# Optimization experiments

Hardware: AMD Instinct MI355X
Metric: run time of the kernel (lower is better)

## Reference

```python
import jax, jax.numpy as jnp
import numpy as np
import math

DIM = 64
N_, H_, W_ = 8, 64, 64
EPS = 1e-5


def setup_inputs() -> dict:
    key = jax.random.key(0)
    ks = jax.random.split(key, 11)
    c = DIM
    s = 1.0 / math.sqrt(c)
    x = jax.random.normal(ks[0], (N_, c, H_, W_), dtype=jnp.float32)
    return {
        "x": x,
        "gamma": jnp.ones((c,), jnp.float32),
        "beta": jnp.zeros((c,), jnp.float32),
        "wq": jax.random.normal(ks[1], (c, c), jnp.float32) * s,
        "bq": jax.random.normal(ks[2], (c,), jnp.float32) * 0.01,
        "wk": jax.random.normal(ks[3], (c, c), jnp.float32) * s,
        "bk": jax.random.normal(ks[4], (c,), jnp.float32) * 0.01,
        "wv": jax.random.normal(ks[5], (c, c), jnp.float32) * s,
        "bv": jax.random.normal(ks[6], (c,), jnp.float32) * 0.01,
        "wo": jax.random.normal(ks[7], (c, c), jnp.float32) * s,
        "bo": jax.random.normal(ks[8], (c,), jnp.float32) * 0.01,
    }


def _conv1x1(x, w, b):
    # 1x1 conv == channel mixing: x [n,c,h,w], w [out,in], b [out]
    return jnp.einsum('nchw,oc->nohw', x, w) + b[None, :, None, None]


def _batchnorm(x, gamma, beta):
    # training-mode BatchNorm2d: biased batch stats over (N,H,W)
    mean = jnp.mean(x, axis=(0, 2, 3), keepdims=True)
    var = jnp.var(x, axis=(0, 2, 3), keepdims=True)
    xn = (x - mean) * jax.lax.rsqrt(var + EPS)
    return xn * gamma[None, :, None, None] + beta[None, :, None, None]


def reference(x, gamma, beta, wq, bq, wk, bk, wv, bv, wo, bo):
    n, c, h, w = x.shape
    hw = h * w
    norm_x = _batchnorm(x, gamma, beta)
    q = _conv1x1(norm_x, wq, bq).reshape(n, c, hw)  # [n,c,hw]
    k = _conv1x1(norm_x, wk, bk).reshape(n, c, hw)  # [n,c,hw]
    v = _conv1x1(norm_x, wv, bv).reshape(n, c, hw)  # [n,c,hw]
    # scores [n, hw, hw] = q^T k / sqrt(c) -- full N x N matrix (memory bound)
    scores = jnp.einsum('nci,ncj->nij', q, k) / math.sqrt(c)
    attn = jax.nn.softmax(scores, axis=-1)
    # res [n, hw, c] = attn @ v^T
    res = jnp.einsum('nij,ncj->nic', attn, v)
    # faithful to original: raw reshape [n,hw,c] -> [n,c,h,w] (no transpose)
    res = res.reshape(n, c, h, w)
    res = _conv1x1(res, wo, bo)
    return x + res
```

## Files before the change

### kernel.cpp

```cpp
#include <hip/hip_runtime.h>


#define HW 4096
#define CC 64
#define NBATCH 8
#define SPLIT 2
#define TSTEPS 32
#define QSCALE 0.18033688011112042f

using f32x4 = __attribute__((ext_vector_type(4))) float;
using bf16x8 = __attribute__((ext_vector_type(8))) short;
using u32x2 = __attribute__((ext_vector_type(2))) unsigned int;
typedef unsigned short u16;
typedef unsigned int u32;

#if __has_builtin(__builtin_amdgcn_exp2f)
#define EXP2F(v) __builtin_amdgcn_exp2f(v)
#else
#define EXP2F(v) exp2f(v)
#endif

#define MFMA16(a, b, c) __builtin_amdgcn_mfma_f32_16x16x32_bf16(a, b, c, 0, 0, 0)
#define GLDS(gsrc, ldst)                                              \
  __builtin_amdgcn_global_load_lds(                                   \
      (const __attribute__((address_space(1))) void*)(gsrc),          \
      (__attribute__((address_space(3))) void*)(ldst), 16, 0, 0)

__device__ __forceinline__ u16 f2bf(float v) {
  u32 u = __float_as_uint(v);
  return (u16)((u + 0x7fffu + ((u >> 16) & 1u)) >> 16);
}
__device__ __forceinline__ float bf2f(u16 h) {
  return __uint_as_float(((u32)h) << 16);
}
__device__ __forceinline__ u32 cvtpk_bf16(float lo, float hi) {
  u32 r;
  asm("v_cvt_pk_bf16_f32 %0, %1, %2" : "=v"(r) : "v"(lo), "v"(hi));
  return r;
}

__global__ __launch_bounds__(256) void k_stats1(const float* __restrict__ x,
                                                float* __restrict__ SACC) {
  const int n = blockIdx.x >> 6;
  const int c = blockIdx.x & 63;
  const int tid = threadIdx.x;
  const float* xp = x + ((size_t)n * CC + c) * HW;
  float s1 = 0.f, s2 = 0.f;
#pragma unroll
  for (int i = tid; i < HW; i += 256) {
    const float v = xp[i];
    s1 += v;
    s2 += v * v;
  }
#pragma unroll
  for (int m = 1; m <= 32; m <<= 1) {
    s1 += __shfl_xor(s1, m);
    s2 += __shfl_xor(s2, m);
  }
  __shared__ float r1[4], r2[4];
  const int w = tid >> 6;
  if ((tid & 63) == 0) { r1[w] = s1; r2[w] = s2; }
  __syncthreads();
  if (tid == 0) {
    unsafeAtomicAdd(SACC + c, r1[0] + r1[1] + r1[2] + r1[3]);
    unsafeAtomicAdd(SACC + CC + c, r2[0] + r2[1] + r2[2] + r2[3]);
  }
}

__device__ __forceinline__ void mm16(const float* __restrict__ W,
                                     const float* __restrict__ B,
                                     const float* xcol, int o0, float scale,
                                     float* outv) {
#pragma unroll
  for (int oo = 0; oo < 16; ++oo) {
    const int o = o0 + oo;
    float a = B[o];
#pragma unroll
    for (int c = 0; c < CC; ++c) a = fmaf(W[o * CC + c], xcol[c], a);
    outv[oo] = a * scale;
  }
}

__device__ __forceinline__ void split_store16(const float* v16, u16* dh, u16* dl) {
  u32 hi[8], lo[8];
#pragma unroll
  for (int e = 0; e < 8; ++e) {
    const u16 h0 = f2bf(v16[2 * e]), h1 = f2bf(v16[2 * e + 1]);
    const float l0 = v16[2 * e] - bf2f(h0);
    const float l1 = v16[2 * e + 1] - bf2f(h1);
    hi[e] = (u32)h0 | ((u32)h1 << 16);
    lo[e] = (u32)f2bf(l0) | ((u32)f2bf(l1) << 16);
  }
  ((uint4*)dh)[0] = *(const uint4*)&hi[0];
  ((uint4*)dh)[1] = *(const uint4*)&hi[4];
  ((uint4*)dl)[0] = *(const uint4*)&lo[0];
  ((uint4*)dl)[1] = *(const uint4*)&lo[4];
}

__global__ __launch_bounds__(256) void k_qkv(
    const float* __restrict__ x, const float* __restrict__ SACC,
    const float* __restrict__ gamma, const float* __restrict__ beta,
    const float* __restrict__ wq, const float* __restrict__ bq,
    const float* __restrict__ wk, const float* __restrict__ bk,
    const float* __restrict__ wv, const float* __restrict__ bv,
    u16* __restrict__ QH, u16* __restrict__ QL, u16* __restrict__ KH,
    u16* __restrict__ KL, u16* __restrict__ V) {
  const int n = blockIdx.x >> 6;
  const int i0 = (blockIdx.x & 63) << 6;
  __shared__ float xn[CC][64];
  __shared__ float sa[CC], sb[CC];
  const int tid = threadIdx.x;
  if (tid < CC) {
    const float inv = 1.0f / (float)(NBATCH * HW);
    const float mean = SACC[tid] * inv;
    const float var = SACC[CC + tid] * inv - mean * mean;
    const float a = rsqrtf(var + 1e-5f) * gamma[tid];
    sa[tid] = a;
    sb[tid] = beta[tid] - mean * a;
  }
  __syncthreads();
  {
    const int p = tid & 63;
    const int c0 = (tid >> 6) << 4;
    const float* xp = x + (size_t)n * CC * HW + i0 + p;
#pragma unroll
    for (int cc = 0; cc < 16; ++cc) {
      const int c = c0 + cc;
      xn[c][p] = fmaf(xp[(size_t)c * HW], sa[c], sb[c]);
    }
  }
  __syncthreads();
  const int w = __builtin_amdgcn_readfirstlane(tid >> 6);
  const int p = tid & 63;
  float xcol[CC];
#pragma unroll
  for (int c = 0; c < CC; ++c) xcol[c] = xn[c][p];

  const size_t row = (size_t)n * HW + i0 + p;
  float v16[16];
  mm16(wq, bq, xcol, w * 16, QSCALE, v16);
  split_store16(v16, QH + row * CC + w * 16, QL + row * CC + w * 16);
  mm16(wk, bk, xcol, w * 16, 1.0f, v16);
  split_store16(v16, KH + row * CC + w * 16, KL + row * CC + w * 16);
  mm16(wv, bv, xcol, w * 16, 1.0f, v16);
#pragma unroll
  for (int oo = 0; oo < 16; ++oo)
    V[((size_t)n * CC + w * 16 + oo) * HW + i0 + p] = f2bf(v16[oo]);
}

__global__ __launch_bounds__(256, 2) void k_attn(
    const u16* __restrict__ QH, const u16* __restrict__ QL,
    const u16* __restrict__ KH, const u16* __restrict__ KL,
    const u16* __restrict__ V, float* __restrict__ RES,
    float* __restrict__ Z) {
  const int bid = blockIdx.x;
  const int n = bid & 7;
  const int qt = (bid >> 3) & 31;
  const int s = bid >> 8;
  const int tid = threadIdx.x;
  const int w = tid >> 6;
  const int l = tid & 63;
  const int l15 = l & 15;
  const int lg = l >> 4;
  const int qw0 = qt * 128 + w * 32;
  const int key0 = s * (TSTEPS * 64);

  __shared__ alignas(16) u16 KHs[2][64][64];
  __shared__ alignas(16) u16 KLs[2][64][64];
  __shared__ alignas(16) u16 Vs[2][64][64];
  __shared__ alignas(16) u16 P[4][32][64];

  const int lr8 = l >> 3;
  const u32 eoff = (u32)(((l & 7) * 8) ^ (lr8 << 3));
  const u16* sp[6];
  u16* d0[6];
  u16* d1[6];
  size_t stp[6];
#pragma unroll
  for (int c = 0; c < 6; ++c) {
    const int idx = w * 6 + c;
    const int tile = idx >> 3;
    const int j = idx & 7;
    const int lrow = j * 8 + lr8;
    if (tile == 0) {
      sp[c] = KH + ((size_t)n * HW + key0 + lrow) * CC + eoff;
      stp[c] = (size_t)64 * CC;
      d0[c] = &KHs[0][j * 8][0];
      d1[c] = &KHs[1][j * 8][0];
    } else if (tile == 1) {
      sp[c] = KL + ((size_t)n * HW + key0 + lrow) * CC + eoff;
      stp[c] = (size_t)64 * CC;
      d0[c] = &KLs[0][j * 8][0];
      d1[c] = &KLs[1][j * 8][0];
    } else {
      sp[c] = V + ((size_t)n * CC + lrow) * HW + key0 + eoff;
      stp[c] = 64;
      d0[c] = &Vs[0][j * 8][0];
      d1[c] = &Vs[1][j * 8][0];
    }
  }
  auto stage = [&](int bufsel) {
#pragma unroll
    for (int c = 0; c < 6; ++c) {
      u16* dst = bufsel ? d1[c] : d0[c];
      GLDS(sp[c], dst);
      sp[c] += stp[c];
    }
  };

  bf16x8 qh[2][2], ql[2][2];
  {
    const size_t qbase = ((size_t)n * HW + qw0 + l15) * CC + lg * 8;
#pragma unroll
    for (int qb = 0; qb < 2; ++qb)
#pragma unroll
      for (int m = 0; m < 2; ++m) {
        const size_t off = qbase + (size_t)qb * 16 * CC + m * 32;
        qh[qb][m] = *(const bf16x8*)(QH + off);
        ql[qb][m] = *(const bf16x8*)(QL + off);
      }
  }

  f32x4 acc[2][4];
#pragma unroll
  for (int qb = 0; qb < 2; ++qb)
#pragma unroll
    for (int chb = 0; chb < 4; ++chb)
      acc[qb][chb] = (f32x4){0.f, 0.f, 0.f, 0.f};
  float zacc[2] = {0.f, 0.f};

  stage(0);
  asm volatile("s_waitcnt vmcnt(0)\n\ts_barrier" ::: "memory");

  const int swz = (l15 & 7) << 4;
  char* const Pw = (char*)&P[w][0][0];

#pragma unroll 1
  for (int t = 0; t < TSTEPS; ++t) {
    const int buf = t & 1;
    if (t + 1 < TSTEPS) stage(buf ^ 1);
    const char* khb = (const char*)&KHs[buf][0][0];
    const char* klb = (const char*)&KLs[buf][0][0];
    const char* vsb = (const char*)&Vs[buf][0][0];

    f32x4 sc[2][4];
#pragma unroll
    for (int kb = 0; kb < 4; ++kb) {
      const int rb = (kb * 16 + l15) * 128;
      const int c0 = (lg * 16) ^ swz;
      const int c1 = (64 + lg * 16) ^ swz;
      const bf16x8 kh0 = *(const bf16x8*)(khb + rb + c0);
      const bf16x8 kh1 = *(const bf16x8*)(khb + rb + c1);
      const bf16x8 kl0 = *(const bf16x8*)(klb + rb + c0);
      const bf16x8 kl1 = *(const bf16x8*)(klb + rb + c1);
      __builtin_amdgcn_s_setprio(1);
#pragma unroll
      for (int qb = 0; qb < 2; ++qb) {
        f32x4 s4 = {0.f, 0.f, 0.f, 0.f};
        s4 = MFMA16(kh0, qh[qb][0], s4);
        s4 = MFMA16(kh1, qh[qb][1], s4);
        s4 = MFMA16(kh0, ql[qb][0], s4);
        s4 = MFMA16(kh1, ql[qb][1], s4);
        s4 = MFMA16(kl0, qh[qb][0], s4);
        s4 = MFMA16(kl1, qh[qb][1], s4);
        sc[qb][kb] = s4;
      }
      __builtin_amdgcn_s_setprio(0);
    }
#pragma unroll
    for (int qb = 0; qb < 2; ++qb) {
      char* const prow = Pw + (qb * 16 + l15) * 128;
      float zs = 0.f;
#pragma unroll
      for (int kb = 0; kb < 4; ++kb) {
        const float p0 = EXP2F(sc[qb][kb][0]);
        const float p1 = EXP2F(sc[qb][kb][1]);
        const float p2 = EXP2F(sc[qb][kb][2]);
        const float p3 = EXP2F(sc[qb][kb][3]);
        zs += (p0 + p1) + (p2 + p3);
        const u32x2 pk = {cvtpk_bf16(p0, p1), cvtpk_bf16(p2, p3)};
        *(u32x2*)(prow + ((kb * 32 + lg * 8) ^ swz)) = pk;
      }
      zacc[qb] += zs;
    }
#pragma unroll
    for (int m2 = 0; m2 < 2; ++m2) {
      const int cc2 = (m2 * 64 + lg * 16) ^ swz;
      bf16x8 vb[4];
#pragma unroll
      for (int chb = 0; chb < 4; ++chb)
        vb[chb] = *(const bf16x8*)(vsb + (chb * 16 + l15) * 128 + cc2);
      __builtin_amdgcn_s_setprio(1);
#pragma unroll
      for (int qb = 0; qb < 2; ++qb) {
        const bf16x8 pa = *(const bf16x8*)(Pw + (qb * 16 + l15) * 128 + cc2);
#pragma unroll
        for (int chb = 0; chb < 4; ++chb)
          acc[qb][chb] = MFMA16(pa, vb[chb], acc[qb][chb]);
      }
      __builtin_amdgcn_s_setprio(0);
    }
    asm volatile("s_waitcnt vmcnt(0) lgkmcnt(0)\n\ts_barrier" ::: "memory");
  }

#pragma unroll
  for (int qb = 0; qb < 2; ++qb) {
    zacc[qb] += __shfl_xor(zacc[qb], 16);
    zacc[qb] += __shfl_xor(zacc[qb], 32);
  }
  if (l < 16) {
    unsafeAtomicAdd(Z + (size_t)n * HW + qw0 + l, zacc[0]);
    unsafeAtomicAdd(Z + (size_t)n * HW + qw0 + 16 + l, zacc[1]);
  }
  float* resn = RES + ((size_t)n * HW + qw0) * CC;
#pragma unroll
  for (int qb = 0; qb < 2; ++qb)
#pragma unroll
    for (int r = 0; r < 4; ++r) {
      const int row = qb * 16 + lg * 4 + r;
#pragma unroll
      for (int chb = 0; chb < 4; ++chb)
        unsafeAtomicAdd(resn + (size_t)row * CC + chb * 16 + l15,
                        acc[qb][chb][r]);
    }
}

__global__ __launch_bounds__(256) void k_out(const float* __restrict__ RES,
                                             const float* __restrict__ Z,
                                             const float* __restrict__ x,
                                             const float* __restrict__ wo,
                                             const float* __restrict__ bo,
                                             float* __restrict__ out) {
  const int n = blockIdx.x >> 6;
  const int j = ((blockIdx.x & 63) << 6) + (threadIdx.x & 63);
  const int oq = __builtin_amdgcn_readfirstlane(threadIdx.x >> 6);
  const float* rn = RES + (size_t)n * HW * CC;
  const float* zb = Z + (size_t)n * HW;
  const int jh = j >> 6;
  float rcol[CC];
#pragma unroll
  for (int c2 = 0; c2 < CC; ++c2)
    rcol[c2] = rn[(size_t)c2 * HW + j] * (1.0f / zb[c2 * 64 + jh]);
  const size_t xb = (size_t)n * CC * HW;
  for (int o = oq * 16; o < oq * 16 + 16; ++o) {
    float sacc = bo[o];
#pragma unroll
    for (int c2 = 0; c2 < CC; ++c2)
      sacc = fmaf(wo[o * CC + c2], rcol[c2], sacc);
    out[xb + (size_t)o * HW + j] = x[xb + (size_t)o * HW + j] + sacc;
  }
}

extern "C" void kernel_launch(void* const* d_in, const int* in_sizes, int n_in,
                              void* d_out, int out_size, void* d_ws,
                              size_t ws_size, hipStream_t stream) {
  const float* x = (const float*)d_in[0];
  const float* gamma = (const float*)d_in[1];
  const float* beta = (const float*)d_in[2];
  const float* wq = (const float*)d_in[3];
  const float* bq = (const float*)d_in[4];
  const float* wk = (const float*)d_in[5];
  const float* bk = (const float*)d_in[6];
  const float* wv = (const float*)d_in[7];
  const float* bv = (const float*)d_in[8];
  const float* wo = (const float*)d_in[9];
  const float* bo = (const float*)d_in[10];
  float* out = (float*)d_out;

  char* ws = (char*)d_ws;
  float* SACC = (float*)ws;
  float* Z = (float*)(ws + 1024);
  float* RES = (float*)(ws + 1024 + (size_t)NBATCH * HW * 4);
  const size_t INIT_BYTES =
      1024 + (size_t)NBATCH * HW * 4 + (size_t)NBATCH * HW * CC * 4;
  const size_t ARR = (size_t)NBATCH * HW * CC;
  u16* QH = (u16*)(ws + INIT_BYTES);
  u16* QL = QH + ARR;
  u16* KH = QL + ARR;
  u16* KL = KH + ARR;
  u16* V = KL + ARR;

  hipMemsetAsync(ws, 0, INIT_BYTES, stream);
  hipLaunchKernelGGL(k_stats1, dim3(512), dim3(256), 0, stream, x, SACC);
  hipLaunchKernelGGL(k_qkv, dim3(512), dim3(256), 0, stream, x, SACC, gamma,
                     beta, wq, bq, wk, bk, wv, bv, QH, QL, KH, KL, V);
  hipLaunchKernelGGL(k_attn, dim3(512), dim3(256), 0, stream, QH, QL, KH, KL,
                     V, RES, Z);
  hipLaunchKernelGGL(k_out, dim3(512), dim3(256), 0, stream, RES, Z, x, wo, bo,
                     out);
}
```

Baseline: 232.1 us.

## Split attention keys four ways, load V directly to registers, coalesce QK stores

Splits the key range into four chunks instead of two, which doubles the attention grid to 1024 blocks and raises the occupancy target to three blocks per SM. V tiles are now loaded straight from global memory into registers rather than staged through shared memory, which frees LDS and drops the V staging work. In the QKV kernel, the Q/K hi/lo values are transposed through shared memory so each row is written with coalesced 16-byte stores. The costs are more atomic traffic on Z and RES partial sums, and exposed global-load latency for V inside the loop.

```diff
diff --git a/kernel.cpp b/kernel.cpp
--- a/kernel.cpp
+++ b/kernel.cpp
@@ -4,8 +4,8 @@
 #define HW 4096
 #define CC 64
 #define NBATCH 8
-#define SPLIT 2
-#define TSTEPS 32
+#define SPLIT 4
+#define TSTEPS 16
 #define QSCALE 0.18033688011112042f
 
 using f32x4 = __attribute__((ext_vector_type(4))) float;
@@ -79,22 +79,6 @@
     for (int c = 0; c < CC; ++c) a = fmaf(W[o * CC + c], xcol[c], a);
     outv[oo] = a * scale;
   }
-}
-
-__device__ __forceinline__ void split_store16(const float* v16, u16* dh, u16* dl) {
-  u32 hi[8], lo[8];
-#pragma unroll
-  for (int e = 0; e < 8; ++e) {
-    const u16 h0 = f2bf(v16[2 * e]), h1 = f2bf(v16[2 * e + 1]);
-    const float l0 = v16[2 * e] - bf2f(h0);
-    const float l1 = v16[2 * e + 1] - bf2f(h1);
-    hi[e] = (u32)h0 | ((u32)h1 << 16);
-    lo[e] = (u32)f2bf(l0) | ((u32)f2bf(l1) << 16);
-  }
-  ((uint4*)dh)[0] = *(const uint4*)&hi[0];
-  ((uint4*)dh)[1] = *(const uint4*)&hi[4];
-  ((uint4*)dl)[0] = *(const uint4*)&lo[0];
-  ((uint4*)dl)[1] = *(const uint4*)&lo[4];
 }
 
 __global__ __launch_bounds__(256) void k_qkv(
@@ -109,6 +93,8 @@
   const int i0 = (blockIdx.x & 63) << 6;
   __shared__ float xn[CC][64];
   __shared__ float sa[CC], sb[CC];
+  __shared__ u16 TH[64][68];
+  __shared__ u16 TL[64][68];
   const int tid = threadIdx.x;
   if (tid < CC) {
     const float inv = 1.0f / (float)(NBATCH * HW);
@@ -136,19 +122,55 @@
 #pragma unroll
   for (int c = 0; c < CC; ++c) xcol[c] = xn[c][p];
 
-  const size_t row = (size_t)n * HW + i0 + p;
+  const size_t rowbase = (size_t)n * HW + i0;
+  u32* const th32 = (u32*)&TH[0][0];
+  u32* const tl32 = (u32*)&TL[0][0];
+  const int wb32 = (p * 68 + w * 16) >> 1;
+  const int r = tid >> 2;
+  const int q4 = tid & 3;
+  const int rb32 = (r * 68 + q4 * 16) >> 1;
+
   float v16[16];
-  mm16(wq, bq, xcol, w * 16, QSCALE, v16);
-  split_store16(v16, QH + row * CC + w * 16, QL + row * CC + w * 16);
-  mm16(wk, bk, xcol, w * 16, 1.0f, v16);
-  split_store16(v16, KH + row * CC + w * 16, KL + row * CC + w * 16);
+#pragma unroll
+  for (int conv = 0; conv < 2; ++conv) {
+    if (conv == 0)
+      mm16(wq, bq, xcol, w * 16, QSCALE, v16);
+    else
+      mm16(wk, bk, xcol, w * 16, 1.0f, v16);
+#pragma unroll
+    for (int e = 0; e < 8; ++e) {
+      const float v0 = v16[2 * e], v1 = v16[2 * e + 1];
+      const u16 h0 = f2bf(v0), h1 = f2bf(v1);
+      th32[wb32 + e] = (u32)h0 | ((u32)h1 << 16);
+      tl32[wb32 + e] =
+          (u32)f2bf(v0 - bf2f(h0)) | ((u32)f2bf(v1 - bf2f(h1)) << 16);
+    }
+    __syncthreads();
+    {
+      u16* const dh = (conv == 0 ? QH : KH) + (rowbase + r) * CC + q4 * 16;
+      u16* const dl = (conv == 0 ? QL : KL) + (rowbase + r) * CC + q4 * 16;
+      const u32x2 a0 = *(const u32x2*)&th32[rb32];
+      const u32x2 a1 = *(const u32x2*)&th32[rb32 + 2];
+      const u32x2 a2 = *(const u32x2*)&th32[rb32 + 4];
+      const u32x2 a3 = *(const u32x2*)&th32[rb32 + 6];
+      *(uint4*)dh = make_uint4(a0[0], a0[1], a1[0], a1[1]);
+      *(uint4*)(dh + 8) = make_uint4(a2[0], a2[1], a3[0], a3[1]);
+      const u32x2 b0 = *(const u32x2*)&tl32[rb32];
+      const u32x2 b1 = *(const u32x2*)&tl32[rb32 + 2];
+      const u32x2 b2 = *(const u32x2*)&tl32[rb32 + 4];
+      const u32x2 b3 = *(const u32x2*)&tl32[rb32 + 6];
+      *(uint4*)dl = make_uint4(b0[0], b0[1], b1[0], b1[1]);
+      *(uint4*)(dl + 8) = make_uint4(b2[0], b2[1], b3[0], b3[1]);
+    }
+    __syncthreads();
+  }
   mm16(wv, bv, xcol, w * 16, 1.0f, v16);
 #pragma unroll
   for (int oo = 0; oo < 16; ++oo)
     V[((size_t)n * CC + w * 16 + oo) * HW + i0 + p] = f2bf(v16[oo]);
 }
 
-__global__ __launch_bounds__(256, 2) void k_attn(
+__global__ __launch_bounds__(256, 3) void k_attn(
     const u16* __restrict__ QH, const u16* __restrict__ QL,
     const u16* __restrict__ KH, const u16* __restrict__ KL,
     const u16* __restrict__ V, float* __restrict__ RES,
@@ -167,44 +189,34 @@
 
   __shared__ alignas(16) u16 KHs[2][64][64];
   __shared__ alignas(16) u16 KLs[2][64][64];
-  __shared__ alignas(16) u16 Vs[2][64][64];
   __shared__ alignas(16) u16 P[4][32][64];
 
   const int lr8 = l >> 3;
   const u32 eoff = (u32)(((l & 7) * 8) ^ (lr8 << 3));
-  const u16* sp[6];
-  u16* d0[6];
-  u16* d1[6];
-  size_t stp[6];
-#pragma unroll
-  for (int c = 0; c < 6; ++c) {
-    const int idx = w * 6 + c;
+  const u16* sp[4];
+  u16* d0[4];
+  u16* d1[4];
+#pragma unroll
+  for (int c = 0; c < 4; ++c) {
+    const int idx = w * 4 + c;
     const int tile = idx >> 3;
     const int j = idx & 7;
     const int lrow = j * 8 + lr8;
     if (tile == 0) {
       sp[c] = KH + ((size_t)n * HW + key0 + lrow) * CC + eoff;
-      stp[c] = (size_t)64 * CC;
       d0[c] = &KHs[0][j * 8][0];
       d1[c] = &KHs[1][j * 8][0];
-    } else if (tile == 1) {
+    } else {
       sp[c] = KL + ((size_t)n * HW + key0 + lrow) * CC + eoff;
-      stp[c] = (size_t)64 * CC;
       d0[c] = &KLs[0][j * 8][0];
       d1[c] = &KLs[1][j * 8][0];
-    } else {
-      sp[c] = V + ((size_t)n * CC + lrow) * HW + key0 + eoff;
-      stp[c] = 64;
-      d0[c] = &Vs[0][j * 8][0];
-      d1[c] = &Vs[1][j * 8][0];
     }
   }
   auto stage = [&](int bufsel) {
 #pragma unroll
-    for (int c = 0; c < 6; ++c) {
-      u16* dst = bufsel ? d1[c] : d0[c];
-      GLDS(sp[c], dst);
-      sp[c] += stp[c];
+    for (int c = 0; c < 4; ++c) {
+      GLDS(sp[c], bufsel ? d1[c] : d0[c]);
+      sp[c] += (size_t)64 * CC;
     }
   };
 
@@ -229,6 +241,8 @@
       acc[qb][chb] = (f32x4){0.f, 0.f, 0.f, 0.f};
   float zacc[2] = {0.f, 0.f};
 
+  const u16* vp = V + ((size_t)n * CC + l15) * HW + key0 + lg * 8;
+
   stage(0);
   asm volatile("s_waitcnt vmcnt(0)\n\ts_barrier" ::: "memory");
 
@@ -238,10 +252,16 @@
 #pragma unroll 1
   for (int t = 0; t < TSTEPS; ++t) {
     const int buf = t & 1;
+    bf16x8 vb[2][4];
+#pragma unroll
+    for (int m2 = 0; m2 < 2; ++m2)
+#pragma unroll
+      for (int chb = 0; chb < 4; ++chb)
+        vb[m2][chb] =
+            *(const bf16x8*)(vp + (size_t)chb * 16 * HW + m2 * 32);
     if (t + 1 < TSTEPS) stage(buf ^ 1);
     const char* khb = (const char*)&KHs[buf][0][0];
     const char* klb = (const char*)&KLs[buf][0][0];
-    const char* vsb = (const char*)&Vs[buf][0][0];
 
     f32x4 sc[2][4];
 #pragma unroll
@@ -285,21 +305,18 @@
     }
 #pragma unroll
     for (int m2 = 0; m2 < 2; ++m2) {
-      const int cc2 = (m2 * 64 + lg * 16) ^ swz;
-      bf16x8 vb[4];
-#pragma unroll
-      for (int chb = 0; chb < 4; ++chb)
-        vb[chb] = *(const bf16x8*)(vsb + (chb * 16 + l15) * 128 + cc2);
       __builtin_amdgcn_s_setprio(1);
 #pragma unroll
       for (int qb = 0; qb < 2; ++qb) {
-        const bf16x8 pa = *(const bf16x8*)(Pw + (qb * 16 + l15) * 128 + cc2);
+        const bf16x8 pa = *(const bf16x8*)(
+            Pw + (qb * 16 + l15) * 128 + ((m2 * 64 + lg * 16) ^ swz));
 #pragma unroll
         for (int chb = 0; chb < 4; ++chb)
-          acc[qb][chb] = MFMA16(pa, vb[chb], acc[qb][chb]);
+          acc[qb][chb] = MFMA16(pa, vb[m2][chb], acc[qb][chb]);
       }
       __builtin_amdgcn_s_setprio(0);
     }
+    vp += 64;
     asm volatile("s_waitcnt vmcnt(0) lgkmcnt(0)\n\ts_barrier" ::: "memory");
   }
 
@@ -384,7 +401,7 @@
   hipLaunchKernelGGL(k_stats1, dim3(512), dim3(256), 0, stream, x, SACC);
   hipLaunchKernelGGL(k_qkv, dim3(512), dim3(256), 0, stream, x, SACC, gamma,
                      beta, wq, bq, wk, bk, wv, bv, QH, QL, KH, KL, V);
-  hipLaunchKernelGGL(k_attn, dim3(512), dim3(256), 0, stream, QH, QL, KH, KL,
+  hipLaunchKernelGGL(k_attn, dim3(1024), dim3(256), 0, stream, QH, QL, KH, KL,
                      V, RES, Z);
   hipLaunchKernelGGL(k_out, dim3(512), dim3(256), 0, stream, RES, Z, x, wo, bo,
                      out);
```

After: 300.9 us. 29.7% more time.
